# Kernel optimization log

Hardware: AMD Instinct MI355X
Metric: run time of the kernel (lower is better)

## Reference

```python
import jax, jax.numpy as jnp
import numpy as np

# Static configuration (matches init_kwargs)
EMBED_DIM = 256
NUM_HEADS = 8
NUM_LEVELS = 4
NUM_POINTS = 16
N_DEGREE = 3
HEAD_DIM = EMBED_DIM // NUM_HEADS
SPATIAL_SHAPES = ((64, 64), (32, 32), (16, 16), (8, 8))  # (H, W) per level
LEN_V = sum(h * w for h, w in SPATIAL_SHAPES)


def _bilinear_gather(v, loc, Hl, Wl):
    """Bilinear sampling with zero padding, align_corners=False.
    v:   [bs, nH, Hl*Wl, hd]  flattened level feature map (per head)
    loc: [bs, nH, Q, 2]       (x, y) in [0, 1]
    returns [bs, nH, Q, hd]
    """
    x = loc[..., 0] * Wl - 0.5
    y = loc[..., 1] * Hl - 0.5
    x0 = jnp.floor(x)
    y0 = jnp.floor(y)
    wx = x - x0
    wy = y - y0
    out = jnp.zeros(v.shape[:2] + (loc.shape[2], v.shape[-1]), v.dtype)
    corners = ((0, 0, (1 - wx) * (1 - wy)), (1, 0, wx * (1 - wy)),
               (0, 1, (1 - wx) * wy), (1, 1, wx * wy))
    for dx, dy, w in corners:
        xi = x0 + dx
        yi = y0 + dy
        valid = (xi >= 0) & (xi < Wl) & (yi >= 0) & (yi < Hl)
        idx = (jnp.clip(yi, 0, Hl - 1) * Wl + jnp.clip(xi, 0, Wl - 1)).astype(jnp.int32)
        g = jnp.take_along_axis(v, idx[..., None], axis=2)  # [bs,nH,Q,hd]
        out = out + g * (w * valid.astype(w.dtype))[..., None]
    return out


def setup_inputs() -> dict:
    key = jax.random.key(0)
    ks = jax.random.split(key, 12)
    bs, Lq = 4, 1024
    s = 0.02
    return {
        "query": jax.random.normal(ks[0], (bs, Lq, EMBED_DIM), jnp.float32),
        # polynomial coefficients for x(l), y(l); scaled so curves stay roughly in [0,1]
        "reference_points": jax.random.uniform(ks[1], (bs, Lq, 2 * (N_DEGREE + 1)), jnp.float32) * 0.25,
        "value": jax.random.normal(ks[2], (bs, LEN_V, EMBED_DIM), jnp.float32),
        "W_value": jax.random.normal(ks[3], (EMBED_DIM, EMBED_DIM), jnp.float32) * s,
        "b_value": jnp.zeros((EMBED_DIM,), jnp.float32),
        "W_offsets": jax.random.normal(ks[4], (EMBED_DIM, NUM_HEADS * NUM_LEVELS * NUM_POINTS * 2), jnp.float32) * s,
        "b_offsets": jax.random.normal(ks[5], (NUM_HEADS * NUM_LEVELS * NUM_POINTS * 2,), jnp.float32) * 0.5,
        "W_attn": jax.random.normal(ks[6], (EMBED_DIM, NUM_HEADS * NUM_LEVELS * NUM_POINTS), jnp.float32) * s,
        "b_attn": jnp.zeros((NUM_HEADS * NUM_LEVELS * NUM_POINTS,), jnp.float32),
        "W_out": jax.random.normal(ks[7], (EMBED_DIM, EMBED_DIM), jnp.float32) * s,
        "b_out": jnp.zeros((EMBED_DIM,), jnp.float32),
    }


def reference(query, reference_points, value, W_value, b_value, W_offsets,
              b_offsets, W_attn, b_attn, W_out, b_out):
    bs, Lq, _ = query.shape
    Lv = value.shape[1]
    nH, nL, nP, hd = NUM_HEADS, NUM_LEVELS, NUM_POINTS, HEAD_DIM

    v = (value @ W_value + b_value).reshape(bs, Lv, nH, hd)

    sampling_offsets = (query @ W_offsets + b_offsets).reshape(bs, Lq, nH, nL, nP, 2)
    attn = jax.nn.softmax((query @ W_attn + b_attn).reshape(bs, Lq, nH, nL * nP), axis=-1)
    attn = attn.reshape(bs, Lq, nH, nL, nP)

    # reference_points last dim == 8: polynomial branch
    lambdaz = jnp.linspace(0.0, 1.0, nP)
    lambdas = jnp.stack([lambdaz ** i for i in range(N_DEGREE, -1, -1)], axis=1)  # [nP, deg+1]
    ref_polys = reference_points.reshape(bs, Lq, 2, N_DEGREE + 1)
    pnts = jnp.einsum('bqcd,pd->bqpc', ref_polys, lambdas)  # [bs,Lq,nP,2] (x,y)

    # offset_normalizer: spatial shapes flipped -> (W, H) per level
    normalizer = jnp.array([[w, h] for (h, w) in SPATIAL_SHAPES], jnp.float32)
    normalizer = normalizer.reshape(1, 1, 1, nL, 1, 2)
    sampling_locations = pnts[:, :, None, None, :, :] + sampling_offsets / normalizer
    # -> [bs, Lq, nH, nL, nP, 2] in [0,1]

    # deformable attention core: per-level bilinear gather + softmax-weighted sum
    out = jnp.zeros((bs, Lq, nH, hd), v.dtype)
    start = 0
    for lvl, (Hl, Wl) in enumerate(SPATIAL_SHAPES):
        v_l = v[:, start:start + Hl * Wl].transpose(0, 2, 1, 3)  # [bs,nH,Hl*Wl,hd]
        loc_l = sampling_locations[:, :, :, lvl]                 # [bs,Lq,nH,nP,2]
        loc_l = loc_l.transpose(0, 2, 1, 3, 4).reshape(bs, nH, Lq * nP, 2)
        sampled = _bilinear_gather(v_l, loc_l, Hl, Wl).reshape(bs, nH, Lq, nP, hd)
        out = out + jnp.einsum('bhqpd,bqhp->bqhd', sampled, attn[:, :, :, lvl])
        start += Hl * Wl

    output = out.reshape(bs, Lq, nH * hd) @ W_out + b_out
    return output, sampling_locations, attn
```

## Files before the change

### kernel.cpp

```cpp
#include <hip/hip_runtime.h>
#include <math.h>

#define BS 4
#define LQ 1024
#define EMB 256
#define NH 8
#define NL 4
#define NP 16
#define HD 32
#define LV 5440
#define LVP 5936
#define KDIM 256

typedef __attribute__((ext_vector_type(8))) short short8;
typedef __attribute__((ext_vector_type(4))) float f32x4;

__device__ inline unsigned short f2bf(float f) {
    unsigned u = __builtin_bit_cast(unsigned, f);
    u += 0x7fff + ((u >> 16) & 1);
    return (unsigned short)(u >> 16);
}


__global__ __launch_bounds__(256) void prep(const float* __restrict__ Wv,
                                            const float* __restrict__ Wo,
                                            const float* __restrict__ Wa,
                                            const float* __restrict__ Wu,
                                            const float* __restrict__ value,
                                            const float* __restrict__ query,
                                            unsigned short* __restrict__ Wt,
                                            unsigned short* __restrict__ val_bf,
                                            unsigned short* __restrict__ qry_bf,
                                            unsigned short* __restrict__ v_pad) {
    const int blk = blockIdx.x;
    const int t = threadIdx.x;
    if (blk < 512) {
        __shared__ float tile[32][33];
        const int n0 = (blk & 63) * 32, k0 = (blk >> 6) * 32;
        const float* src; int N, nloc;
        if (n0 < 256)       { src = Wv; N = 256;  nloc = n0; }
        else if (n0 < 1280) { src = Wo; N = 1024; nloc = n0 - 256; }
        else if (n0 < 1792) { src = Wa; N = 512;  nloc = n0 - 1280; }
        else                { src = Wu; N = 256;  nloc = n0 - 1792; }
        const int tx = t & 31, ty = t >> 5;
#pragma unroll
        for (int i = 0; i < 32; i += 8)
            tile[ty + i][tx] = src[(size_t)(k0 + ty + i) * N + nloc + tx];
        __syncthreads();
        if (t < 128) {
            const int n_loc = t & 31, oct = t >> 5;
            const int n = n0 + n_loc;
            short8 h;
#pragma unroll
            for (int e = 0; e < 8; ++e) h[e] = (short)f2bf(tile[oct * 8 + e][n_loc]);
            const size_t off = ((size_t)(n >> 4) * 8 + (k0 >> 5)) * 512
                             + ((n & 15) + 16 * oct) * 8;
            *(short8*)(Wt + off) = h;
        }
    } else if (blk < 3744) {
        int i; const float* src; unsigned short* dst;
        if (blk < 3232) { i = (blk - 512) * 256 + t;  src = value; dst = val_bf; }
        else            { i = (blk - 3232) * 256 + t; src = query; dst = qry_bf; }
        const int r = i >> 5, oct = i & 31, k0 = oct * 8;
        const float4 f0 = *(const float4*)(src + (size_t)r * KDIM + k0);
        const float4 f1 = *(const float4*)(src + (size_t)r * KDIM + k0 + 4);
        short8 h;
        h[0] = (short)f2bf(f0.x); h[1] = (short)f2bf(f0.y);
        h[2] = (short)f2bf(f0.z); h[3] = (short)f2bf(f0.w);
        h[4] = (short)f2bf(f1.x); h[5] = (short)f2bf(f1.y);
        h[6] = (short)f2bf(f1.z); h[7] = (short)f2bf(f1.w);
        const size_t off = ((size_t)(r >> 4) * 8 + (oct >> 2)) * 512
                         + ((r & 15) + 16 * (oct & 3)) * 8;
        *(short8*)(dst + off) = h;
    } else {
        const int pidx = (blk - 3744) * 8 + (t >> 5);
        const int lane32 = t & 31;
        const unsigned b = (unsigned)pidx / 496u;
        const unsigned rem = (unsigned)pidx - b * 496u;
        int Wd, W2, pb, i;
        if (rem < 260)      { Wd = 64; W2 = 66; pb = 0;    i = rem; }
        else if (rem < 392) { Wd = 32; W2 = 34; pb = 4356; i = rem - 260; }
        else if (rem < 460) { Wd = 16; W2 = 18; pb = 5512; i = rem - 392; }
        else                { Wd = 8;  W2 = 10; pb = 5836; i = rem - 460; }
        int y, x;
        if (i < W2)          { y = 0;      x = i; }
        else if (i < 2 * W2) { y = Wd + 1; x = i - W2; }
        else { const int j = i - 2 * W2; y = 1 + (j >> 1); x = (j & 1) ? (Wd + 1) : 0; }
        const size_t off = ((size_t)b * LVP + pb + y * W2 + x) * EMB + lane32 * 8;
        uint4 z = {0, 0, 0, 0};
        *(uint4*)(v_pad + off) = z;
    }
}

template <int MODE>
__device__ __forceinline__ void gemm_nolds(const unsigned short* __restrict__ A,
                                           const unsigned short* __restrict__ Bt,
                                           const float* __restrict__ bias,
                                           const float* __restrict__ bias2,
                                           const float* __restrict__ refp,
                                           void* __restrict__ Cv,
                                           float* __restrict__ C2,
                                           int N, int bx, int by) {
    const int t = threadIdx.x;
    const int lane = t & 63, w = t >> 6;
    const int quad = lane >> 4, l16 = lane & 15;
    const int wr = w >> 1, wc = w & 1;
    const int row0 = by * 128, col0 = bx * 128;

    const unsigned short* ap = A  + ((size_t)((row0 >> 4) + wr * 4) * 8) * 512 + lane * 8;
    const unsigned short* bp = Bt + ((size_t)((col0 >> 4) + wc * 4) * 8) * 512 + lane * 8;

    f32x4 acc[4][4] = {};

#pragma unroll 2
    for (int kt = 0; kt < 8; ++kt) {
        short8 af[4], bf[4];
#pragma unroll
        for (int mi = 0; mi < 4; ++mi)
            af[mi] = *(const short8*)(ap + (size_t)mi * 4096 + kt * 512);
#pragma unroll
        for (int ni = 0; ni < 4; ++ni)
            bf[ni] = *(const short8*)(bp + (size_t)ni * 4096 + kt * 512);
#pragma unroll
        for (int mi = 0; mi < 4; ++mi)
#pragma unroll
            for (int ni = 0; ni < 4; ++ni)
                acc[mi][ni] = __builtin_amdgcn_mfma_f32_16x16x32_bf16(af[mi], bf[ni],
                                                                      acc[mi][ni], 0, 0, 0);
    }

    if (MODE == 0) {
#pragma unroll
        for (int ni = 0; ni < 4; ++ni) {
            const int c = col0 + wc * 64 + ni * 16 + l16;
            const float bv = bias[c];
#pragma unroll
            for (int mi = 0; mi < 4; ++mi) {
                const int r0 = row0 + wr * 64 + mi * 16 + quad * 4;
#pragma unroll
                for (int rr = 0; rr < 4; ++rr)
                    ((float*)Cv)[(size_t)(r0 + rr) * N + c] = acc[mi][ni][rr] + bv;
            }
        }
    } else if (MODE == 2) {
        unsigned short* C = (unsigned short*)Cv;
        float bv[4];
        int cc[4];
#pragma unroll
        for (int ni = 0; ni < 4; ++ni) {
            cc[ni] = col0 + wc * 64 + ni * 16 + l16;
            bv[ni] = bias[cc[ni]];
        }
#pragma unroll
        for (int mi = 0; mi < 4; ++mi) {
#pragma unroll
            for (int rr = 0; rr < 4; ++rr) {
                const unsigned r = row0 + wr * 64 + mi * 16 + quad * 4 + rr;
                const unsigned b = r / 5440u;
                const unsigned flat = r - b * 5440u;
                unsigned y, x, W2, pb;
                if (flat < 4096)      { y = flat >> 6; x = flat & 63; W2 = 66; pb = 0; }
                else if (flat < 5120) { const unsigned f = flat - 4096; y = f >> 5; x = f & 31; W2 = 34; pb = 4356; }
                else if (flat < 5376) { const unsigned f = flat - 5120; y = f >> 4; x = f & 15; W2 = 18; pb = 5512; }
                else                  { const unsigned f = flat - 5376; y = f >> 3; x = f & 7;  W2 = 10; pb = 5836; }
                const size_t rowbase = ((size_t)b * LVP + pb + (y + 1) * W2 + (x + 1)) * EMB;
#pragma unroll
                for (int ni = 0; ni < 4; ++ni)
                    C[rowbase + cc[ni]] = f2bf(acc[mi][ni][rr] + bv[ni]);
            }
        }
    } else {
        const bool is_off = (col0 < 1024);
        if (is_off) {
            float* C = (float*)Cv;
#pragma unroll
            for (int ni = 0; ni < 4; ++ni) {
                const int cg = col0 + wc * 64 + ni * 16 + l16;
                const int xy = cg & 1, p = (cg >> 1) & 15, l = (cg >> 5) & 3;
                const float lam = (float)p * (1.0f / 15.0f);
                const float l2 = lam * lam, l3 = l2 * lam;
                const float rW = (l == 0) ? 0.015625f : (l == 1) ? 0.03125f
                                : (l == 2) ? 0.0625f : 0.125f;
                const float bv = bias[cg];
#pragma unroll
                for (int mi = 0; mi < 4; ++mi) {
                    const int r0 = row0 + wr * 64 + mi * 16 + quad * 4;
#pragma unroll
                    for (int rr = 0; rr < 4; ++rr) {
                        const int r = r0 + rr;
                        const float4 rp = *(const float4*)(refp + (size_t)r * 8 + xy * 4);
                        const float poly = rp.x * l3 + rp.y * l2 + rp.z * lam + rp.w;
                        C[(size_t)r * 1024 + cg] = poly + (acc[mi][ni][rr] + bv) * rW;
                    }
                }
            }
        } else {
            const int cabase = col0 - 1024 + wc * 64;
            float bv[4];
#pragma unroll
            for (int ni = 0; ni < 4; ++ni) bv[ni] = bias2[cabase + ni * 16 + l16];
#pragma unroll
            for (int mi = 0; mi < 4; ++mi) {
                const int r0 = row0 + wr * 64 + mi * 16 + quad * 4;
#pragma unroll
                for (int rr = 0; rr < 4; ++rr) {
                    float v0 = acc[mi][0][rr] + bv[0];
                    float v1 = acc[mi][1][rr] + bv[1];
                    float v2 = acc[mi][2][rr] + bv[2];
                    float v3 = acc[mi][3][rr] + bv[3];
                    float mx = fmaxf(fmaxf(v0, v1), fmaxf(v2, v3));
#pragma unroll
                    for (int mk = 1; mk < 16; mk <<= 1) mx = fmaxf(mx, __shfl_xor(mx, mk));
                    v0 = __expf(v0 - mx); v1 = __expf(v1 - mx);
                    v2 = __expf(v2 - mx); v3 = __expf(v3 - mx);
                    float s = v0 + v1 + v2 + v3;
#pragma unroll
                    for (int mk = 1; mk < 16; mk <<= 1) s += __shfl_xor(s, mk);
                    const float inv = 1.0f / s;
                    const size_t rb = (size_t)(r0 + rr) * 512 + cabase + l16;
                    C2[rb]      = v0 * inv;
                    C2[rb + 16] = v1 * inv;
                    C2[rb + 32] = v2 * inv;
                    C2[rb + 48] = v3 * inv;
                }
            }
        }
    }
}

__global__ __launch_bounds__(256, 2) void gemm_fused(const unsigned short* __restrict__ val_bf,
                                                     const unsigned short* __restrict__ qry_bf,
                                                     const unsigned short* __restrict__ Wt,
                                                     const float* __restrict__ b_value,
                                                     const float* __restrict__ b_off,
                                                     const float* __restrict__ b_attn,
                                                     const float* __restrict__ refp,
                                                     unsigned short* __restrict__ v_pad,
                                                     float* __restrict__ loc_out,
                                                     float* __restrict__ attn_out) {
    const int b = blockIdx.x;
    if (b < 340) {
        gemm_nolds<2>(val_bf, Wt, b_value, nullptr, nullptr,
                      v_pad, nullptr, 256, b & 1, b >> 1);
    } else {
        const int b2 = b - 340;
        gemm_nolds<1>(qry_bf, Wt + (size_t)256 * KDIM, b_off, b_attn, refp,
                      loc_out, attn_out, 1536, b2 % 12, b2 / 12);
    }
}

__global__ __launch_bounds__(256, 2) void gemm_outp(const unsigned short* __restrict__ interm,
                                                    const unsigned short* __restrict__ Wt_out,
                                                    const float* __restrict__ b_out,
                                                    float* __restrict__ out) {
    gemm_nolds<0>(interm, Wt_out, b_out, nullptr, nullptr,
                  out, nullptr, 256, blockIdx.x & 1, blockIdx.x >> 1);
}

__global__ __launch_bounds__(256, 4) void sample_kernel(const unsigned short* __restrict__ v,
                                                        const float* __restrict__ loc,
                                                        const float* __restrict__ attn,
                                                        unsigned short* __restrict__ interm) {
    const int t = threadIdx.x;
    const int g = blockIdx.x * 16 + (t >> 4);
    const int l16i = t & 15;
    const int lvl = l16i >> 2;
    const int cq  = l16i & 3;
    const int h = g & 7, bq = g >> 3, b = bq >> 10;

    const int Wd = 64 >> lvl;
    const float Wf = (float)Wd;
    const int W2 = Wd + 2;
    const int rowoff = W2 * EMB;
    const int pb = (lvl == 0) ? 0 : (lvl == 1) ? 4356 : (lvl == 2) ? 5512 : 5836;

    const float* lp = loc  + (size_t)g * 128 + lvl * 32;
    const float* ap = attn + (size_t)g * 64  + lvl * 16;
    const unsigned short* vl = v + ((size_t)b * LVP + pb) * EMB + h * HD + cq * 8;

    float2 acc2[4] = {};

    auto cvt2 = [](unsigned d) {
        uint2 u; u.x = d << 16; u.y = d & 0xffff0000u;
        return __builtin_bit_cast(float2, u);
    };
    auto cadd = [&](const uint4 q, float wgt) {
        const float2 w2 = make_float2(wgt, wgt);
        acc2[0] += cvt2(q.x) * w2;
        acc2[1] += cvt2(q.y) * w2;
        acc2[2] += cvt2(q.z) * w2;
        acc2[3] += cvt2(q.w) * w2;
    };

    auto point = [&](float lx, float ly, float wt) {
        const float x = fmaf(lx, Wf, -0.5f);
        const float y = fmaf(ly, Wf, -0.5f);
        const float xc = fminf(fmaxf(x, -1.0f), Wf);
        const float yc = fminf(fmaxf(y, -1.0f), Wf);
        const float x0f = fminf(floorf(xc), Wf - 1.0f);
        const float y0f = fminf(floorf(yc), Wf - 1.0f);
        const float wx = xc - x0f, wy = yc - y0f;
        const float iwx = 1.0f - wx, iwy = 1.0f - wy;
        const int px = (int)x0f + 1;
        const int py = (int)y0f + 1;
        const int base = (py * W2 + px) * EMB;
        const float w00 = iwx * iwy * wt, w10 = wx * iwy * wt;
        const float w01 = iwx * wy * wt,  w11 = wx * wy * wt;
        const uint4 g00 = *(const uint4*)(vl + base);
        const uint4 g10 = *(const uint4*)(vl + base + EMB);
        const uint4 g01 = *(const uint4*)(vl + base + rowoff);
        const uint4 g11 = *(const uint4*)(vl + base + rowoff + EMB);
        cadd(g00, w00); cadd(g10, w10); cadd(g01, w01); cadd(g11, w11);
    };

#pragma unroll 1
    for (int p4 = 0; p4 < 16; p4 += 4) {
        const float4 la = *(const float4*)(lp + 2 * p4);
        const float4 lb = *(const float4*)(lp + 2 * p4 + 4);
        const float4 wv = *(const float4*)(ap + p4);
        point(la.x, la.y, wv.x); point(la.z, la.w, wv.y);
        point(lb.x, lb.y, wv.z); point(lb.z, lb.w, wv.w);
    }

    float a[8] = {acc2[0].x, acc2[0].y, acc2[1].x, acc2[1].y,
                  acc2[2].x, acc2[2].y, acc2[3].x, acc2[3].y};
#pragma unroll
    for (int m = 4; m <= 8; m <<= 1)
#pragma unroll
        for (int k = 0; k < 8; ++k) a[k] += __shfl_xor(a[k], m);

    if (lvl == 0) {
        unsigned short o[8];
#pragma unroll
        for (int k = 0; k < 8; ++k) o[k] = f2bf(a[k]);
        const size_t off = ((size_t)(bq >> 4) * 8 + h) * 512
                         + ((bq & 15) + 16 * cq) * 8;
        *(uint4*)(interm + off) = *(const uint4*)o;
    }
}

extern "C" void kernel_launch(void* const* d_in, const int* in_sizes, int n_in,
                              void* d_out, int out_size, void* d_ws, size_t ws_size,
                              hipStream_t stream) {
    const float* query   = (const float*)d_in[0];
    const float* refp    = (const float*)d_in[1];
    const float* value   = (const float*)d_in[2];
    const float* W_value = (const float*)d_in[3];
    const float* b_value = (const float*)d_in[4];
    const float* W_off   = (const float*)d_in[5];
    const float* b_off   = (const float*)d_in[6];
    const float* W_attn  = (const float*)d_in[7];
    const float* b_attn  = (const float*)d_in[8];
    const float* W_out   = (const float*)d_in[9];
    const float* b_out   = (const float*)d_in[10];

    float* out      = (float*)d_out;
    float* loc_out  = out + 1048576;
    float* attn_out = out + 5242880;

    char* ws = (char*)d_ws;
    unsigned short* v_pad  = (unsigned short*)ws;
    unsigned short* val_bf = (unsigned short*)(ws + 12156928);
    unsigned short* interm = (unsigned short*)(ws + 12156928);
    unsigned short* qry_bf = (unsigned short*)(ws + 23298048);
    unsigned short* Wt_all = (unsigned short*)(ws + 25395200);

    const dim3 blk(256);

    prep<<<3992, blk, 0, stream>>>(W_value, W_off, W_attn, W_out, value, query,
                                   Wt_all, val_bf, qry_bf, v_pad);

    gemm_fused<<<724, blk, 0, stream>>>(val_bf, qry_bf, Wt_all, b_value, b_off,
                                        b_attn, refp, v_pad, loc_out, attn_out);

    sample_kernel<<<(BS * LQ * NH) / 16, blk, 0, stream>>>(v_pad, loc_out, attn_out, interm);

    gemm_outp<<<64, blk, 0, stream>>>(interm, Wt_all + (size_t)1792 * KDIM, b_out, out);
}
```

Baseline: 165.6 us.

## Switch bf16 pipeline to fp16 with packed half FMA in sampling

Changes all intermediate storage and MFMA from bf16 to fp16, using hardware conversion instead of manual rounding. The sampling kernel now accumulates in packed half2 multiply-adds instead of unpacking to float2, roughly halving the ALU work per gathered corner. The prep kernel's activation conversion is restructured so each wave handles a 16-row group across all k tiles, which needs far fewer blocks. The trade-off is that fp16 accumulation over 64 weighted samples loses precision and may overflow where bf16 would not.

```diff
diff --git a/kernel.cpp b/kernel.cpp
--- a/kernel.cpp
+++ b/kernel.cpp
@@ -12,13 +12,15 @@
 #define LVP 5936
 #define KDIM 256
 
-typedef __attribute__((ext_vector_type(8))) short short8;
+typedef _Float16 half8 __attribute__((ext_vector_type(8)));
+typedef _Float16 h2    __attribute__((ext_vector_type(2)));
 typedef __attribute__((ext_vector_type(4))) float f32x4;
 
-__device__ inline unsigned short f2bf(float f) {
-    unsigned u = __builtin_bit_cast(unsigned, f);
-    u += 0x7fff + ((u >> 16) & 1);
-    return (unsigned short)(u >> 16);
+__device__ inline unsigned short f2h(float f) {
+    return __builtin_bit_cast(unsigned short, (_Float16)f);
+}
+__device__ inline h2 pk2(float f) {
+    return __builtin_bit_cast(h2, __builtin_amdgcn_cvt_pkrtz(f, f));
 }
 
 
@@ -29,8 +31,8 @@
                                             const float* __restrict__ value,
                                             const float* __restrict__ query,
                                             unsigned short* __restrict__ Wt,
-                                            unsigned short* __restrict__ val_bf,
-                                            unsigned short* __restrict__ qry_bf,
+                                            unsigned short* __restrict__ val_h,
+                                            unsigned short* __restrict__ qry_h,
                                             unsigned short* __restrict__ v_pad) {
     const int blk = blockIdx.x;
     const int t = threadIdx.x;
@@ -50,30 +52,34 @@
         if (t < 128) {
             const int n_loc = t & 31, oct = t >> 5;
             const int n = n0 + n_loc;
-            short8 h;
-#pragma unroll
-            for (int e = 0; e < 8; ++e) h[e] = (short)f2bf(tile[oct * 8 + e][n_loc]);
+            unsigned short h[8];
+#pragma unroll
+            for (int e = 0; e < 8; ++e) h[e] = f2h(tile[oct * 8 + e][n_loc]);
             const size_t off = ((size_t)(n >> 4) * 8 + (k0 >> 5)) * 512
                              + ((n & 15) + 16 * oct) * 8;
-            *(short8*)(Wt + off) = h;
-        }
-    } else if (blk < 3744) {
-        int i; const float* src; unsigned short* dst;
-        if (blk < 3232) { i = (blk - 512) * 256 + t;  src = value; dst = val_bf; }
-        else            { i = (blk - 3232) * 256 + t; src = query; dst = qry_bf; }
-        const int r = i >> 5, oct = i & 31, k0 = oct * 8;
-        const float4 f0 = *(const float4*)(src + (size_t)r * KDIM + k0);
-        const float4 f1 = *(const float4*)(src + (size_t)r * KDIM + k0 + 4);
-        short8 h;
-        h[0] = (short)f2bf(f0.x); h[1] = (short)f2bf(f0.y);
-        h[2] = (short)f2bf(f0.z); h[3] = (short)f2bf(f0.w);
-        h[4] = (short)f2bf(f1.x); h[5] = (short)f2bf(f1.y);
-        h[6] = (short)f2bf(f1.z); h[7] = (short)f2bf(f1.w);
-        const size_t off = ((size_t)(r >> 4) * 8 + (oct >> 2)) * 512
-                         + ((r & 15) + 16 * (oct & 3)) * 8;
-        *(short8*)(dst + off) = h;
+            *(uint4*)(Wt + off) = *(const uint4*)h;
+        }
+    } else if (blk < 916) {
+        const int u = (blk - 512) * 4 + (t >> 6);
+        const int lane = t & 63;
+        const float* src; unsigned short* dst; int rg;
+        if (u < 1360) { src = value; dst = val_h; rg = u; }
+        else          { src = query; dst = qry_h; rg = u - 1360; }
+        const int r = rg * 16 + (lane & 15);
+        const int quad = lane >> 4;
+        const float* sp = src + (size_t)r * KDIM + quad * 8;
+        unsigned short* dp = dst + (size_t)rg * 4096 + lane * 8;
+#pragma unroll
+        for (int kt = 0; kt < 8; ++kt) {
+            const float4 f0 = *(const float4*)(sp + kt * 32);
+            const float4 f1 = *(const float4*)(sp + kt * 32 + 4);
+            unsigned short h[8];
+            h[0] = f2h(f0.x); h[1] = f2h(f0.y); h[2] = f2h(f0.z); h[3] = f2h(f0.w);
+            h[4] = f2h(f1.x); h[5] = f2h(f1.y); h[6] = f2h(f1.z); h[7] = f2h(f1.w);
+            *(uint4*)(dp + kt * 512) = *(const uint4*)h;
+        }
     } else {
-        const int pidx = (blk - 3744) * 8 + (t >> 5);
+        const int pidx = (blk - 916) * 8 + (t >> 5);
         const int lane32 = t & 31;
         const unsigned b = (unsigned)pidx / 496u;
         const unsigned rem = (unsigned)pidx - b * 496u;
@@ -114,19 +120,19 @@
 
 #pragma unroll 2
     for (int kt = 0; kt < 8; ++kt) {
-        short8 af[4], bf[4];
+        half8 af[4], bf[4];
 #pragma unroll
         for (int mi = 0; mi < 4; ++mi)
-            af[mi] = *(const short8*)(ap + (size_t)mi * 4096 + kt * 512);
+            af[mi] = *(const half8*)(ap + (size_t)mi * 4096 + kt * 512);
 #pragma unroll
         for (int ni = 0; ni < 4; ++ni)
-            bf[ni] = *(const short8*)(bp + (size_t)ni * 4096 + kt * 512);
+            bf[ni] = *(const half8*)(bp + (size_t)ni * 4096 + kt * 512);
 #pragma unroll
         for (int mi = 0; mi < 4; ++mi)
 #pragma unroll
             for (int ni = 0; ni < 4; ++ni)
-                acc[mi][ni] = __builtin_amdgcn_mfma_f32_16x16x32_bf16(af[mi], bf[ni],
-                                                                      acc[mi][ni], 0, 0, 0);
+                acc[mi][ni] = __builtin_amdgcn_mfma_f32_16x16x32_f16(af[mi], bf[ni],
+                                                                     acc[mi][ni], 0, 0, 0);
     }
 
     if (MODE == 0) {
@@ -166,7 +172,7 @@
                 const size_t rowbase = ((size_t)b * LVP + pb + (y + 1) * W2 + (x + 1)) * EMB;
 #pragma unroll
                 for (int ni = 0; ni < 4; ++ni)
-                    C[rowbase + cc[ni]] = f2bf(acc[mi][ni][rr] + bv[ni]);
+                    C[rowbase + cc[ni]] = f2h(acc[mi][ni][rr] + bv[ni]);
             }
         }
     } else {
@@ -228,8 +234,8 @@
     }
 }
 
-__global__ __launch_bounds__(256, 2) void gemm_fused(const unsigned short* __restrict__ val_bf,
-                                                     const unsigned short* __restrict__ qry_bf,
+__global__ __launch_bounds__(256, 2) void gemm_fused(const unsigned short* __restrict__ val_h,
+                                                     const unsigned short* __restrict__ qry_h,
                                                      const unsigned short* __restrict__ Wt,
                                                      const float* __restrict__ b_value,
                                                      const float* __restrict__ b_off,
@@ -240,11 +246,11 @@
                                                      float* __restrict__ attn_out) {
     const int b = blockIdx.x;
     if (b < 340) {
-        gemm_nolds<2>(val_bf, Wt, b_value, nullptr, nullptr,
+        gemm_nolds<2>(val_h, Wt, b_value, nullptr, nullptr,
                       v_pad, nullptr, 256, b & 1, b >> 1);
     } else {
         const int b2 = b - 340;
-        gemm_nolds<1>(qry_bf, Wt + (size_t)256 * KDIM, b_off, b_attn, refp,
+        gemm_nolds<1>(qry_h, Wt + (size_t)256 * KDIM, b_off, b_attn, refp,
                       loc_out, attn_out, 1536, b2 % 12, b2 / 12);
     }
 }
@@ -278,18 +284,13 @@
     const float* ap = attn + (size_t)g * 64  + lvl * 16;
     const unsigned short* vl = v + ((size_t)b * LVP + pb) * EMB + h * HD + cq * 8;
 
-    float2 acc2[4] = {};
-
-    auto cvt2 = [](unsigned d) {
-        uint2 u; u.x = d << 16; u.y = d & 0xffff0000u;
-        return __builtin_bit_cast(float2, u);
-    };
-    auto cadd = [&](const uint4 q, float wgt) {
-        const float2 w2 = make_float2(wgt, wgt);
-        acc2[0] += cvt2(q.x) * w2;
-        acc2[1] += cvt2(q.y) * w2;
-        acc2[2] += cvt2(q.z) * w2;
-        acc2[3] += cvt2(q.w) * w2;
+    h2 acc2[4] = {};
+
+    auto cadd = [&](const uint4 q, h2 w) {
+        acc2[0] += __builtin_bit_cast(h2, q.x) * w;
+        acc2[1] += __builtin_bit_cast(h2, q.y) * w;
+        acc2[2] += __builtin_bit_cast(h2, q.z) * w;
+        acc2[3] += __builtin_bit_cast(h2, q.w) * w;
     };
 
     auto point = [&](float lx, float ly, float wt) {
@@ -310,7 +311,10 @@
         const uint4 g10 = *(const uint4*)(vl + base + EMB);
         const uint4 g01 = *(const uint4*)(vl + base + rowoff);
         const uint4 g11 = *(const uint4*)(vl + base + rowoff + EMB);
-        cadd(g00, w00); cadd(g10, w10); cadd(g01, w01); cadd(g11, w11);
+        cadd(g00, pk2(w00));
+        cadd(g10, pk2(w10));
+        cadd(g01, pk2(w01));
+        cadd(g11, pk2(w11));
     };
 
 #pragma unroll 1
@@ -322,8 +326,12 @@
         point(lb.x, lb.y, wv.z); point(lb.z, lb.w, wv.w);
     }
 
-    float a[8] = {acc2[0].x, acc2[0].y, acc2[1].x, acc2[1].y,
-                  acc2[2].x, acc2[2].y, acc2[3].x, acc2[3].y};
+    float a[8];
+#pragma unroll
+    for (int k = 0; k < 4; ++k) {
+        a[2 * k]     = (float)acc2[k][0];
+        a[2 * k + 1] = (float)acc2[k][1];
+    }
 #pragma unroll
     for (int m = 4; m <= 8; m <<= 1)
 #pragma unroll
@@ -332,7 +340,7 @@
     if (lvl == 0) {
         unsigned short o[8];
 #pragma unroll
-        for (int k = 0; k < 8; ++k) o[k] = f2bf(a[k]);
+        for (int k = 0; k < 8; ++k) o[k] = f2h(a[k]);
         const size_t off = ((size_t)(bq >> 4) * 8 + h) * 512
                          + ((bq & 15) + 16 * cq) * 8;
         *(uint4*)(interm + off) = *(const uint4*)o;
@@ -360,17 +368,17 @@
 
     char* ws = (char*)d_ws;
     unsigned short* v_pad  = (unsigned short*)ws;
-    unsigned short* val_bf = (unsigned short*)(ws + 12156928);
+    unsigned short* val_h  = (unsigned short*)(ws + 12156928);
     unsigned short* interm = (unsigned short*)(ws + 12156928);
-    unsigned short* qry_bf = (unsigned short*)(ws + 23298048);
+    unsigned short* qry_h  = (unsigned short*)(ws + 23298048);
     unsigned short* Wt_all = (unsigned short*)(ws + 25395200);
 
     const dim3 blk(256);
 
-    prep<<<3992, blk, 0, stream>>>(W_value, W_off, W_attn, W_out, value, query,
-                                   Wt_all, val_bf, qry_bf, v_pad);
-
-    gemm_fused<<<724, blk, 0, stream>>>(val_bf, qry_bf, Wt_all, b_value, b_off,
+    prep<<<1164, blk, 0, stream>>>(W_value, W_off, W_attn, W_out, value, query,
+                                   Wt_all, val_h, qry_h, v_pad);
+
+    gemm_fused<<<724, blk, 0, stream>>>(val_h, qry_h, Wt_all, b_value, b_off,
                                         b_attn, refp, v_pad, loc_out, attn_out);
 
     sample_kernel<<<(BS * LQ * NH) / 16, blk, 0, stream>>>(v_pad, loc_out, attn_out, interm);
```

Result: no change. 165.7 us (+0.0%).
